# Optimization experiments

Hardware: AMD Instinct MI355X
Metric: run time of the kernel (lower is better)

The kernel has to match this reference:

```python
import math
import jax, jax.numpy as jnp
import numpy as np

DIM = 1024
DIM_HEAD = 64
NUM_HEAD = 16
HIDDEN = DIM_HEAD * NUM_HEAD  # 1024
B, L = 4, 2048
EPS = 1e-12  # torch F.normalize eps


def rms_norm(x, g):
    # F.normalize(x, dim=-1) * g * sqrt(d): L2-normalize then rescale
    d = x.shape[-1]
    norm = jnp.maximum(jnp.linalg.norm(x, axis=-1, keepdims=True), EPS)
    return x / norm * g * math.sqrt(d)


def setup_inputs() -> dict:
    key = jax.random.key(0)
    ks = jax.random.split(key, 8)
    x = jax.random.normal(ks[0], (B, L, DIM), dtype=jnp.float32)
    # torch Linear init scale ~ 1/sqrt(fan_in)
    s1 = 1.0 / math.sqrt(DIM)
    s2 = 1.0 / math.sqrt(HIDDEN)
    Wqkv = jax.random.uniform(ks[1], (3 * HIDDEN, DIM), minval=-s1, maxval=s1, dtype=jnp.float32)
    bqkv = jax.random.uniform(ks[2], (3 * HIDDEN,), minval=-s1, maxval=s1, dtype=jnp.float32)
    Wout = jax.random.uniform(ks[3], (DIM, HIDDEN), minval=-s2, maxval=s2, dtype=jnp.float32)
    bout = jax.random.uniform(ks[4], (DIM,), minval=-s2, maxval=s2, dtype=jnp.float32)
    g_q = jnp.ones((HIDDEN,), dtype=jnp.float32)
    g_k = jnp.ones((HIDDEN,), dtype=jnp.float32)
    g_out = jnp.ones((DIM,), dtype=jnp.float32)
    return {"x": x, "Wqkv": Wqkv, "bqkv": bqkv, "Wout": Wout, "bout": bout,
            "g_q": g_q, "g_k": g_k, "g_out": g_out}


def reference(x, Wqkv, bqkv, Wout, bout, g_q, g_k, g_out):
    scale = DIM_HEAD ** -0.5
    qkv = x @ Wqkv.T + bqkv  # (b, l, 3*hidden)
    q, k, v = jnp.split(qkv, 3, axis=-1)
    # QK RMSNorm applied over flattened (num_head*d) channel dim
    q = rms_norm(q, g_q)
    k = rms_norm(k, g_k)
    split_heads = lambda t: t.reshape(B, L, NUM_HEAD, DIM_HEAD).transpose(0, 2, 1, 3)
    q, k, v = split_heads(q), split_heads(k), split_heads(v)  # (b, h, l, d)
    q = q * scale
    sim = jnp.einsum('bhld,bhnd->bhln', q, k)
    attn = jax.nn.softmax(sim, axis=-1)
    out = jnp.einsum('bhln,bhnd->bhld', attn, v)  # (b, h, l, d)
    out = out.transpose(0, 2, 1, 3).reshape(B, L, HIDDEN)  # b l (h d)
    out = out @ Wout.T + bout
    return rms_norm(out, g_out)
```

## Files before the change

### kernel.cpp

```cpp
#include <hip/hip_runtime.h>
#include <math.h>

#define DIM       1024
#define DIM_HEAD  64
#define NUM_HEAD  16
#define HIDDEN    1024
#define BATCH     4
#define SEQ       2048
#define ROWS      (BATCH * SEQ)
#define QKV_N     (3 * HIDDEN)
#define QK_N      2048

typedef __bf16 bf16_t;
typedef __bf16 bf16x8 __attribute__((ext_vector_type(8)));
typedef __bf16 bf16x4 __attribute__((ext_vector_type(4)));
typedef float  f32x4  __attribute__((ext_vector_type(4)));

#define F32_ONE_PATTERN 0x3F800000u
#define LOG2E 1.44269504088896f

#define GLOAD_LDS16(gp, lp)                                                  \
    __builtin_amdgcn_global_load_lds(                                        \
        (const __attribute__((address_space(1))) void*)(const void*)(gp),    \
        (__attribute__((address_space(3))) void*)(void*)(lp), 16, 0, 0)

__global__ __launch_bounds__(256) void decode_all(
    const void* __restrict__ x_raw,    const void* __restrict__ wqkv_raw,
    const void* __restrict__ wout_raw, const void* __restrict__ bqkv_raw,
    const void* __restrict__ bout_raw, const void* __restrict__ gq_raw,
    const void* __restrict__ gk_raw,   const void* __restrict__ gout_raw,
    bf16_t* __restrict__ xb, bf16_t* __restrict__ wqkvb, bf16_t* __restrict__ woutb,
    float* __restrict__ o_bqkv, float* __restrict__ o_bout,
    float* __restrict__ o_gq,   float* __restrict__ o_gk,
    float* __restrict__ o_gout,
    const unsigned* __restrict__ sniff)
{
    const bool isf32 = (*sniff == F32_ONE_PATTERN);
    const int blk = blockIdx.x;
    if (blk < 6144) {
        const void* src; bf16_t* dst; long base;
        if (blk < 4096)      { src = x_raw;    dst = xb;    base = (long)blk * 2048; }
        else if (blk < 5632) { src = wqkv_raw; dst = wqkvb; base = (long)(blk - 4096) * 2048; }
        else                 { src = wout_raw; dst = woutb; base = (long)(blk - 5632) * 2048; }
        const long i = base + threadIdx.x * 8;
        if (isf32) {
            const float* p = (const float*)src + i;
            f32x4 a = *(const f32x4*)p;
            f32x4 b = *(const f32x4*)(p + 4);
            bf16x8 r;
            r[0] = (bf16_t)a[0]; r[1] = (bf16_t)a[1]; r[2] = (bf16_t)a[2]; r[3] = (bf16_t)a[3];
            r[4] = (bf16_t)b[0]; r[5] = (bf16_t)b[1]; r[6] = (bf16_t)b[2]; r[7] = (bf16_t)b[3];
            *(bf16x8*)&dst[i] = r;
        } else {
            *(bf16x8*)&dst[i] = *(const bf16x8*)((const bf16_t*)src + i);
        }
    } else {
        const int pb = blk - 6144;
        const void* src; float* dst; int off;
        if (pb < 3)       { src = bqkv_raw; dst = o_bqkv; off = pb * 1024; }
        else if (pb == 3) { src = bout_raw; dst = o_bout; off = 0; }
        else if (pb == 4) { src = gq_raw;   dst = o_gq;   off = 0; }
        else if (pb == 5) { src = gk_raw;   dst = o_gk;   off = 0; }
        else              { src = gout_raw; dst = o_gout; off = 0; }
        const int i = off + threadIdx.x * 4;
        if (isf32) {
            *(f32x4*)&dst[i] = *((const f32x4*)src + (off >> 2) + threadIdx.x);
        } else {
            bf16x4 v = *((const bf16x4*)src + (off >> 2) + threadIdx.x);
            f32x4 a;
            a[0] = (float)v[0]; a[1] = (float)v[1]; a[2] = (float)v[2]; a[3] = (float)v[3];
            *(f32x4*)&dst[i] = a;
        }
    }
}

__global__ __launch_bounds__(256) void gemm_qkv(
    const bf16_t* __restrict__ A,
    const bf16_t* __restrict__ Bt,
    const float*  __restrict__ bias,
    bf16_t* __restrict__ qk,
    bf16_t* __restrict__ vt)
{
    __shared__ __align__(16) bf16_t smem[16384];
    bf16_t* const As = smem;
    bf16_t* const Bs = smem + 8192;
    bf16_t* const Ts = smem;

    const int tid  = threadIdx.x;
    const int w    = tid >> 6;
    const int lane = tid & 63;
    const int wr   = w >> 1;
    const int wc   = w & 1;
    const int lr   = lane & 15;
    const int quad = lane >> 4;

    int lid = blockIdx.y * 24 + blockIdx.x;
    lid = (lid & 7) * 192 + (lid >> 3);
    const int bx = lid % 24, by = lid / 24;
    const int m0 = by * 128;
    const int n0 = bx * 128;
    const int K  = DIM;

    const int r    = tid >> 3;
    const int cswz = (((tid & 7) * 16) ^ ((r & 7) << 4)) >> 1;

    const int fsw0 = (quad * 8) ^ ((lr & 7) << 3);
    const int fsw1 = (32 + quad * 8) ^ ((lr & 7) << 3);

    f32x4 acc[4][4];
    #pragma unroll
    for (int i = 0; i < 4; i++)
        #pragma unroll
        for (int j = 0; j < 4; j++)
            acc[i][j] = (f32x4){0.f, 0.f, 0.f, 0.f};

    const bf16_t* pa = &A [(size_t)(m0 + r) * K + cswz];
    const bf16_t* pb = &Bt[(size_t)(n0 + r) * K + cswz];

    for (int k0 = 0; k0 < K; k0 += 64) {
        __syncthreads();
        #pragma unroll
        for (int p = 0; p < 4; p++) {
            GLOAD_LDS16(pa + (size_t)p * 32 * K + k0, &As[p * 2048 + tid * 8]);
            GLOAD_LDS16(pb + (size_t)p * 32 * K + k0, &Bs[p * 2048 + tid * 8]);
        }
        __syncthreads();

        bf16x8 af0[4], af1[4], bf0[4], bf1[4];
        #pragma unroll
        for (int i = 0; i < 4; i++) {
            const int row = (wr * 64 + i * 16 + lr) * 64;
            af0[i] = *(const bf16x8*)&As[row + fsw0];
            af1[i] = *(const bf16x8*)&As[row + fsw1];
        }
        #pragma unroll
        for (int j = 0; j < 4; j++) {
            const int row = (wc * 64 + j * 16 + lr) * 64;
            bf0[j] = *(const bf16x8*)&Bs[row + fsw0];
            bf1[j] = *(const bf16x8*)&Bs[row + fsw1];
        }
        #pragma unroll
        for (int i = 0; i < 4; i++)
            #pragma unroll
            for (int j = 0; j < 4; j++)
                acc[i][j] = __builtin_amdgcn_mfma_f32_16x16x32_bf16(
                    bf0[j], af0[i], acc[i][j], 0, 0, 0);
        #pragma unroll
        for (int i = 0; i < 4; i++)
            #pragma unroll
            for (int j = 0; j < 4; j++)
                acc[i][j] = __builtin_amdgcn_mfma_f32_16x16x32_bf16(
                    bf1[j], af1[i], acc[i][j], 0, 0, 0);
    }

    if (n0 < 2048) {
        #pragma unroll
        for (int i = 0; i < 4; i++) {
            const int row = m0 + wr * 64 + i * 16 + lr;
            #pragma unroll
            for (int j = 0; j < 4; j++) {
                const int col = n0 + wc * 64 + j * 16 + quad * 4;
                f32x4 bv = *(const f32x4*)&bias[col];
                f32x4 v = acc[i][j];
                bf16x4 o;
                o[0] = (bf16_t)(v[0] + bv[0]);
                o[1] = (bf16_t)(v[1] + bv[1]);
                o[2] = (bf16_t)(v[2] + bv[2]);
                o[3] = (bf16_t)(v[3] + bv[3]);
                *(bf16x4*)&qk[(size_t)row * QK_N + col] = o;
            }
        }
    } else {
        const int b      = m0 >> 11;
        const int l_base = m0 & 2047;
        const int c_base = n0 - 2048;
        #pragma unroll
        for (int p = 0; p < 2; p++) {
            __syncthreads();
            if (wc == p) {
                #pragma unroll
                for (int j = 0; j < 4; j++) {
                    const int cb = j * 16 + quad * 4;
                    f32x4 bv = *(const f32x4*)&bias[2048 + c_base + p * 64 + cb];
                    #pragma unroll
                    for (int i = 0; i < 4; i++) {
                        const int l = wr * 64 + i * 16 + lr;
                        f32x4 v = acc[i][j];
                        #pragma unroll
                        for (int rr = 0; rr < 4; rr++)
                            Ts[(cb + rr) * 136 + l] = (bf16_t)(v[rr] + bv[rr]);
                    }
                }
            }
            __syncthreads();
            const int c2 = tid >> 2, li = (tid & 3) * 32;
            const int cg = c_base + p * 64 + c2;
            const int h = cg >> 6, d = cg & 63;
            bf16_t* vrow = vt + ((size_t)((b << 4) | h) * 64 + d) * SEQ + l_base + li;
            #pragma unroll
            for (int e = 0; e < 4; e++)
                *(bf16x8*)&vrow[e * 8] = *(const bf16x8*)&Ts[c2 * 136 + li + e * 8];
        }
    }
}

__global__ __launch_bounds__(256) void gemm_out(
    const bf16_t* __restrict__ A,
    const bf16_t* __restrict__ Bt,
    const float*  __restrict__ bias,
    bf16_t* __restrict__ C)
{
    __shared__ __align__(16) bf16_t As[128 * 64];
    __shared__ __align__(16) bf16_t Bs[128 * 64];

    const int tid  = threadIdx.x;
    const int w    = tid >> 6;
    const int lane = tid & 63;
    const int wr   = w >> 1;
    const int wc   = w & 1;
    const int lr   = lane & 15;
    const int quad = lane >> 4;

    int lid = blockIdx.y * 8 + blockIdx.x;
    lid = (lid & 7) * 64 + (lid >> 3);
    const int bx = lid & 7, by = lid >> 3;
    const int m0 = by * 128;
    const int n0 = bx * 128;
    const int K  = HIDDEN;
    const int N  = DIM;

    const int r    = tid >> 3;
    const int cswz = (((tid & 7) * 16) ^ ((r & 7) << 4)) >> 1;
    const int fsw0 = (quad * 8) ^ ((lr & 7) << 3);
    const int fsw1 = (32 + quad * 8) ^ ((lr & 7) << 3);

    f32x4 acc[4][4];
    #pragma unroll
    for (int i = 0; i < 4; i++)
        #pragma unroll
        for (int j = 0; j < 4; j++)
            acc[i][j] = (f32x4){0.f, 0.f, 0.f, 0.f};

    const bf16_t* pa = &A [(size_t)(m0 + r) * K + cswz];
    const bf16_t* pb = &Bt[(size_t)(n0 + r) * K + cswz];

    for (int k0 = 0; k0 < K; k0 += 64) {
        __syncthreads();
        #pragma unroll
        for (int p = 0; p < 4; p++) {
            GLOAD_LDS16(pa + (size_t)p * 32 * K + k0, &As[p * 2048 + tid * 8]);
            GLOAD_LDS16(pb + (size_t)p * 32 * K + k0, &Bs[p * 2048 + tid * 8]);
        }
        __syncthreads();

        bf16x8 af0[4], af1[4], bf0[4], bf1[4];
        #pragma unroll
        for (int i = 0; i < 4; i++) {
            const int row = (wr * 64 + i * 16 + lr) * 64;
            af0[i] = *(const bf16x8*)&As[row + fsw0];
            af1[i] = *(const bf16x8*)&As[row + fsw1];
        }
        #pragma unroll
        for (int j = 0; j < 4; j++) {
            const int row = (wc * 64 + j * 16 + lr) * 64;
            bf0[j] = *(const bf16x8*)&Bs[row + fsw0];
            bf1[j] = *(const bf16x8*)&Bs[row + fsw1];
        }
        #pragma unroll
        for (int i = 0; i < 4; i++)
            #pragma unroll
            for (int j = 0; j < 4; j++)
                acc[i][j] = __builtin_amdgcn_mfma_f32_16x16x32_bf16(
                    bf0[j], af0[i], acc[i][j], 0, 0, 0);
        #pragma unroll
        for (int i = 0; i < 4; i++)
            #pragma unroll
            for (int j = 0; j < 4; j++)
                acc[i][j] = __builtin_amdgcn_mfma_f32_16x16x32_bf16(
                    bf1[j], af1[i], acc[i][j], 0, 0, 0);
    }

    #pragma unroll
    for (int i = 0; i < 4; i++) {
        const int row = m0 + wr * 64 + i * 16 + lr;
        #pragma unroll
        for (int j = 0; j < 4; j++) {
            const int col = n0 + wc * 64 + j * 16 + quad * 4;
            f32x4 bv = *(const f32x4*)&bias[col];
            f32x4 v = acc[i][j];
            bf16x4 o;
            o[0] = (bf16_t)(v[0] + bv[0]);
            o[1] = (bf16_t)(v[1] + bv[1]);
            o[2] = (bf16_t)(v[2] + bv[2]);
            o[3] = (bf16_t)(v[3] + bv[3]);
            *(bf16x4*)&C[(size_t)row * N + col] = o;
        }
    }
}

__device__ __forceinline__ void norm_apply(bf16_t* __restrict__ row,
                                           const float* __restrict__ g,
                                           float mult, int tid, float* red)
{
    bf16x4 xv = *(const bf16x4*)&row[tid * 4];
    float f0 = (float)xv[0], f1 = (float)xv[1], f2 = (float)xv[2], f3 = (float)xv[3];
    float ss = f0 * f0 + f1 * f1 + f2 * f2 + f3 * f3;
    #pragma unroll
    for (int off = 32; off > 0; off >>= 1) ss += __shfl_xor(ss, off, 64);
    if ((tid & 63) == 0) red[tid >> 6] = ss;
    __syncthreads();
    const float tot  = red[0] + red[1] + red[2] + red[3];
    const float fac  = mult / fmaxf(sqrtf(tot), 1e-12f);
    f32x4 gv = *(const f32x4*)&g[tid * 4];
    bf16x4 o;
    o[0] = (bf16_t)(f0 * gv[0] * fac);
    o[1] = (bf16_t)(f1 * gv[1] * fac);
    o[2] = (bf16_t)(f2 * gv[2] * fac);
    o[3] = (bf16_t)(f3 * gv[3] * fac);
    *(bf16x4*)&row[tid * 4] = o;
    __syncthreads();
}

__global__ __launch_bounds__(256) void qk_rmsnorm(bf16_t* __restrict__ qk,
                                                  const float* __restrict__ gq,
                                                  const float* __restrict__ gk)
{
    __shared__ float red[4];
    const size_t base = (size_t)blockIdx.x * QK_N;
    norm_apply(qk + base, gq, 4.0f * LOG2E, threadIdx.x, red);
    norm_apply(qk + base + HIDDEN, gk, 32.0f, threadIdx.x, red);
}

__global__ __launch_bounds__(256) void final_rmsnorm(const bf16_t* __restrict__ in,
                                                     const float* __restrict__ g,
                                                     void* __restrict__ out,
                                                     const unsigned* __restrict__ sniff)
{
    __shared__ float red[4];
    const bool isf32 = (*sniff == F32_ONE_PATTERN);
    const int tid = threadIdx.x;
    const bf16_t* row = in + (size_t)blockIdx.x * HIDDEN;

    bf16x4 xv = *(const bf16x4*)&row[tid * 4];
    float f0 = (float)xv[0], f1 = (float)xv[1], f2 = (float)xv[2], f3 = (float)xv[3];
    float ss = f0 * f0 + f1 * f1 + f2 * f2 + f3 * f3;
    #pragma unroll
    for (int off = 32; off > 0; off >>= 1) ss += __shfl_xor(ss, off, 64);
    if ((tid & 63) == 0) red[tid >> 6] = ss;
    __syncthreads();
    const float tot = red[0] + red[1] + red[2] + red[3];
    const float fac = 32.0f / fmaxf(sqrtf(tot), 1e-12f);
    f32x4 gv = *(const f32x4*)&g[tid * 4];
    f32x4 o;
    o[0] = f0 * gv[0] * fac;
    o[1] = f1 * gv[1] * fac;
    o[2] = f2 * gv[2] * fac;
    o[3] = f3 * gv[3] * fac;
    if (isf32) {
        *(f32x4*)((float*)out + (size_t)blockIdx.x * HIDDEN + tid * 4) = o;
    } else {
        bf16x4 ob;
        ob[0] = (bf16_t)o[0]; ob[1] = (bf16_t)o[1];
        ob[2] = (bf16_t)o[2]; ob[3] = (bf16_t)o[3];
        *(bf16x4*)((bf16_t*)out + (size_t)blockIdx.x * HIDDEN + tid * 4) = ob;
    }
}

__global__ __launch_bounds__(256) void attn_mfma9(const bf16_t* __restrict__ qk,
                                                  const bf16_t* __restrict__ vt,
                                                  bf16_t* __restrict__ out)
{
    __shared__ __align__(16) bf16_t Ks[4][2][2048];
    __shared__ __align__(16) union {
        bf16_t Ps[4][64 * 40];
        float  Obuf[2][64][68];
    } sh;
    __shared__ float lred[4][4][16];

    const int tid  = threadIdx.x;
    const int w    = tid >> 6;
    const int lane = tid & 63;
    const int l15  = lane & 15;
    const int quad = lane >> 4;

    const int j    = blockIdx.x;
    const int xcd  = j & 7;
    const int slot = j >> 3;
    const int bh   = ((slot >> 5) << 3) | xcd;
    const int q0   = (slot & 31) * 64;
    const int b = bh >> 4, h = bh & 15;

    bf16x8 qf[4][2];
    #pragma unroll
    for (int qt = 0; qt < 4; qt++) {
        const bf16_t* qrow = qk + (size_t)(b * SEQ + q0 + qt * 16 + l15) * QK_N + h * DIM_HEAD;
        qf[qt][0] = *(const bf16x8*)&qrow[quad * 8];
        qf[qt][1] = *(const bf16x8*)&qrow[32 + quad * 8];
    }

    f32x4 O[4][4];
    float lp[4] = {0.f, 0.f, 0.f, 0.f};
    #pragma unroll
    for (int qt = 0; qt < 4; qt++)
        #pragma unroll
        for (int dt = 0; dt < 4; dt++)
            O[qt][dt] = (f32x4){0.f, 0.f, 0.f, 0.f};

    const int r8  = lane >> 3;
    const int c8l = lane & 7;
    const int srccol = ((c8l * 8 + (r8 & 3) * 16) & 63);
    const bf16_t* kstage = qk + (size_t)(b * SEQ + w * 32) * QK_N + HIDDEN + h * DIM_HEAD
                         + r8 * QK_N + srccol;
    bf16_t* const ksb = &Ks[w][0][0];

    const int swz0 = ((quad * 8 + 64 - (l15 & 3) * 16) & 63);
    const int swz1 = ((32 + quad * 8 + 64 - (l15 & 3) * 16) & 63);
    const int krow = l15 * 64;

    #pragma unroll
    for (int t = 0; t < 4; t++)
        GLOAD_LDS16(kstage + t * 8 * QK_N, ksb + t * 512);
    kstage += 128 * QK_N;

    const bf16_t* vptr = vt + (size_t)bh * 64 * SEQ + w * 32;
    const int voff = l15 * SEQ + quad * 8;
    bf16_t* const psw = sh.Ps[w] + l15 * 40 + quad * 4;
    const bf16_t* const psr = sh.Ps[w] + l15 * 40 + quad * 8;

    for (int it = 0; it < SEQ / 128; it++) {
        const int cur = (it & 1) * 2048;
        const int nxt = 2048 - cur;
        __builtin_amdgcn_s_waitcnt(0x0F70);

        bf16x8 vB[4];
        #pragma unroll
        for (int dt = 0; dt < 4; dt++)
            vB[dt] = *(const bf16x8*)(vptr + voff + dt * 16 * SEQ);
        vptr += 128;

        bf16x8 kA[2][2];
        kA[0][0] = *(const bf16x8*)&ksb[cur + krow + swz0];
        kA[0][1] = *(const bf16x8*)&ksb[cur + krow + swz1];
        kA[1][0] = *(const bf16x8*)&ksb[cur + 1024 + krow + swz0];
        kA[1][1] = *(const bf16x8*)&ksb[cur + 1024 + krow + swz1];

        #pragma unroll
        for (int t = 0; t < 4; t++)
            GLOAD_LDS16(kstage + t * 8 * QK_N, ksb + nxt + t * 512);
        kstage += 128 * QK_N;

        f32x4 s[2][4];
        #pragma unroll
        for (int kt = 0; kt < 2; kt++)
            #pragma unroll
            for (int qt = 0; qt < 4; qt++) {
                f32x4 z = (f32x4){0.f, 0.f, 0.f, 0.f};
                z = __builtin_amdgcn_mfma_f32_16x16x32_bf16(kA[kt][0], qf[qt][0], z, 0, 0, 0);
                s[kt][qt] = __builtin_amdgcn_mfma_f32_16x16x32_bf16(kA[kt][1], qf[qt][1], z, 0, 0, 0);
            }

        #pragma unroll
        for (int qt = 0; qt < 4; qt++)
            #pragma unroll
            for (int kt = 0; kt < 2; kt++) {
                bf16x4 pk;
                #pragma unroll
                for (int r = 0; r < 4; r++) {
                    const float p = __builtin_amdgcn_exp2f(s[kt][qt][r]);
                    lp[qt] += p;
                    pk[r] = (bf16_t)p;
                }
                *(bf16x4*)(psw + qt * 640 + kt * 16) = pk;
            }
        __builtin_amdgcn_s_waitcnt(0xC07F);

        #pragma unroll
        for (int qt = 0; qt < 4; qt++) {
            bf16x8 pf = *(const bf16x8*)(psr + qt * 640);
            #pragma unroll
            for (int dt = 0; dt < 4; dt++)
                O[qt][dt] = __builtin_amdgcn_mfma_f32_16x16x32_bf16(pf, vB[dt], O[qt][dt], 0, 0, 0);
        }
    }

    #pragma unroll
    for (int qt = 0; qt < 4; qt++) {
        lp[qt] += __shfl_xor(lp[qt], 16, 64);
        lp[qt] += __shfl_xor(lp[qt], 32, 64);
    }
    __syncthreads();
    if (w >= 2) {
        #pragma unroll
        for (int qt = 0; qt < 4; qt++)
            #pragma unroll
            for (int dt = 0; dt < 4; dt++)
                #pragma unroll
                for (int r = 0; r < 4; r++)
                    sh.Obuf[w - 2][qt * 16 + quad * 4 + r][dt * 16 + l15] = O[qt][dt][r];
    }
    if (quad == 0) {
        #pragma unroll
        for (int qt = 0; qt < 4; qt++) lred[w][qt][l15] = lp[qt];
    }
    __syncthreads();
    if (w < 2) {
        #pragma unroll
        for (int qt = 0; qt < 4; qt++)
            #pragma unroll
            for (int dt = 0; dt < 4; dt++)
                #pragma unroll
                for (int r = 0; r < 4; r++) {
                    float* p = &sh.Obuf[w][qt * 16 + quad * 4 + r][dt * 16 + l15];
                    *p += O[qt][dt][r];
                }
    }
    __syncthreads();
    #pragma unroll
    for (int i = 0; i < 2; i++) {
        const int u   = tid + i * 256;
        const int row = u >> 3;
        const int c8  = (u & 7) * 8;
        const float ls = lred[0][row >> 4][row & 15] + lred[1][row >> 4][row & 15]
                       + lred[2][row >> 4][row & 15] + lred[3][row >> 4][row & 15];
        const float inv = 1.0f / ls;
        f32x4 a0 = *(const f32x4*)&sh.Obuf[0][row][c8];
        f32x4 a1 = *(const f32x4*)&sh.Obuf[0][row][c8 + 4];
        f32x4 b0 = *(const f32x4*)&sh.Obuf[1][row][c8];
        f32x4 b1 = *(const f32x4*)&sh.Obuf[1][row][c8 + 4];
        bf16x8 o;
        o[0] = (bf16_t)((a0[0] + b0[0]) * inv);
        o[1] = (bf16_t)((a0[1] + b0[1]) * inv);
        o[2] = (bf16_t)((a0[2] + b0[2]) * inv);
        o[3] = (bf16_t)((a0[3] + b0[3]) * inv);
        o[4] = (bf16_t)((a1[0] + b1[0]) * inv);
        o[5] = (bf16_t)((a1[1] + b1[1]) * inv);
        o[6] = (bf16_t)((a1[2] + b1[2]) * inv);
        o[7] = (bf16_t)((a1[3] + b1[3]) * inv);
        *(bf16x8*)&out[(size_t)(b * SEQ + q0 + row) * HIDDEN + h * DIM_HEAD + c8] = o;
    }
}

extern "C" void kernel_launch(void* const* d_in, const int* in_sizes, int n_in,
                              void* d_out, int out_size, void* d_ws, size_t ws_size,
                              hipStream_t stream)
{
    (void)in_sizes; (void)n_in; (void)out_size; (void)ws_size;
    const void* x_raw    = d_in[0];
    const void* Wqkv_raw = d_in[1];
    const void* bqkv_raw = d_in[2];
    const void* Wout_raw = d_in[3];
    const void* bout_raw = d_in[4];
    const void* gq_raw   = d_in[5];
    const void* gk_raw   = d_in[6];
    const void* gout_raw = d_in[7];
    const unsigned* sniff = (const unsigned*)d_in[5];

    char* ws = (char*)d_ws;
    bf16_t* xb      = (bf16_t*)(ws + 0);
    bf16_t* Wqkvb   = (bf16_t*)(ws + (16l << 20));
    bf16_t* Woutb   = (bf16_t*)(ws + (22l << 20));
    float*  bqkv_f  = (float*) (ws + (24l << 20));
    float*  bout_f  = (float*) (ws + (24l << 20) + 16384);
    float*  gq_f    = (float*) (ws + (24l << 20) + 2 * 16384);
    float*  gk_f    = (float*) (ws + (24l << 20) + 3 * 16384);
    float*  gout_f  = (float*) (ws + (24l << 20) + 4 * 16384);
    bf16_t* qk      = (bf16_t*)(ws + (25l << 20));
    bf16_t* vtb     = (bf16_t*)(ws + (57l << 20));
    bf16_t* attn_o  = xb;
    bf16_t* out_b   = qk;

    decode_all<<<6151, 256, 0, stream>>>(
        x_raw, Wqkv_raw, Wout_raw, bqkv_raw, bout_raw, gq_raw, gk_raw, gout_raw,
        xb, Wqkvb, Woutb, bqkv_f, bout_f, gq_f, gk_f, gout_f, sniff);

    gemm_qkv<<<dim3(QKV_N / 128, ROWS / 128), 256, 0, stream>>>(
        xb, Wqkvb, bqkv_f, qk, vtb);
    qk_rmsnorm<<<ROWS, 256, 0, stream>>>(qk, gq_f, gk_f);
    attn_mfma9<<<(SEQ / 64) * BATCH * NUM_HEAD, 256, 0, stream>>>(qk, vtb, attn_o);
    gemm_out<<<dim3(DIM / 128, ROWS / 128), 256, 0, stream>>>(
        attn_o, Woutb, bout_f, out_b);
    final_rmsnorm<<<ROWS, 256, 0, stream>>>(out_b, gout_f, d_out, sniff);
}
```

Baseline: 308.8 us.

## Double-buffer LDS tiles in QKV and output GEMMs to overlap loads with MFMA

Both projection GEMMs now use two LDS buffers (64 KB total) and issue the direct global-to-LDS loads for the next K tile before computing on the current one. Partial vmcnt waits plus raw s_barrier replace the two __syncthreads per iteration, so global memory latency can hide behind the MFMA work. The cost is double the shared memory, which may lower occupancy. It also relies on manual waitcnt counting being correct for the async LDS loads.

```diff
diff --git a/kernel.cpp b/kernel.cpp
--- a/kernel.cpp
+++ b/kernel.cpp
@@ -81,9 +81,7 @@
     bf16_t* __restrict__ qk,
     bf16_t* __restrict__ vt)
 {
-    __shared__ __align__(16) bf16_t smem[16384];
-    bf16_t* const As = smem;
-    bf16_t* const Bs = smem + 8192;
+    __shared__ __align__(16) bf16_t smem[32768];
     bf16_t* const Ts = smem;
 
     const int tid  = threadIdx.x;
@@ -103,7 +101,6 @@
 
     const int r    = tid >> 3;
     const int cswz = (((tid & 7) * 16) ^ ((r & 7) << 4)) >> 1;
-
     const int fsw0 = (quad * 8) ^ ((lr & 7) << 3);
     const int fsw1 = (32 + quad * 8) ^ ((lr & 7) << 3);
 
@@ -117,27 +114,41 @@
     const bf16_t* pa = &A [(size_t)(m0 + r) * K + cswz];
     const bf16_t* pb = &Bt[(size_t)(n0 + r) * K + cswz];
 
-    for (int k0 = 0; k0 < K; k0 += 64) {
-        __syncthreads();
-        #pragma unroll
-        for (int p = 0; p < 4; p++) {
-            GLOAD_LDS16(pa + (size_t)p * 32 * K + k0, &As[p * 2048 + tid * 8]);
-            GLOAD_LDS16(pb + (size_t)p * 32 * K + k0, &Bs[p * 2048 + tid * 8]);
-        }
-        __syncthreads();
+    #pragma unroll
+    for (int p = 0; p < 4; p++) {
+        GLOAD_LDS16(pa + (size_t)p * 32 * K, &smem[p * 2048 + tid * 8]);
+        GLOAD_LDS16(pb + (size_t)p * 32 * K, &smem[8192 + p * 2048 + tid * 8]);
+    }
+
+    const int NT = K / 64;
+    for (int t = 0; t < NT; t++) {
+        const int cur = (t & 1) * 16384;
+        const int nxt = 16384 - cur;
+        if (t + 1 < NT) {
+            const size_t koff = (size_t)(t + 1) * 64;
+            #pragma unroll
+            for (int p = 0; p < 4; p++) {
+                GLOAD_LDS16(pa + (size_t)p * 32 * K + koff, &smem[nxt + p * 2048 + tid * 8]);
+                GLOAD_LDS16(pb + (size_t)p * 32 * K + koff, &smem[nxt + 8192 + p * 2048 + tid * 8]);
+            }
+            asm volatile("s_waitcnt vmcnt(8)" ::: "memory");
+        } else {
+            asm volatile("s_waitcnt vmcnt(0)" ::: "memory");
+        }
+        __builtin_amdgcn_s_barrier();
 
         bf16x8 af0[4], af1[4], bf0[4], bf1[4];
         #pragma unroll
         for (int i = 0; i < 4; i++) {
-            const int row = (wr * 64 + i * 16 + lr) * 64;
-            af0[i] = *(const bf16x8*)&As[row + fsw0];
-            af1[i] = *(const bf16x8*)&As[row + fsw1];
+            const int row = cur + (wr * 64 + i * 16 + lr) * 64;
+            af0[i] = *(const bf16x8*)&smem[row + fsw0];
+            af1[i] = *(const bf16x8*)&smem[row + fsw1];
         }
         #pragma unroll
         for (int j = 0; j < 4; j++) {
-            const int row = (wc * 64 + j * 16 + lr) * 64;
-            bf0[j] = *(const bf16x8*)&Bs[row + fsw0];
-            bf1[j] = *(const bf16x8*)&Bs[row + fsw1];
+            const int row = cur + 8192 + (wc * 64 + j * 16 + lr) * 64;
+            bf0[j] = *(const bf16x8*)&smem[row + fsw0];
+            bf1[j] = *(const bf16x8*)&smem[row + fsw1];
         }
         #pragma unroll
         for (int i = 0; i < 4; i++)
@@ -151,6 +162,7 @@
             for (int j = 0; j < 4; j++)
                 acc[i][j] = __builtin_amdgcn_mfma_f32_16x16x32_bf16(
                     bf1[j], af1[i], acc[i][j], 0, 0, 0);
+        __builtin_amdgcn_s_barrier();
     }
 
     if (n0 < 2048) {
@@ -210,8 +222,7 @@
     const float*  __restrict__ bias,
     bf16_t* __restrict__ C)
 {
-    __shared__ __align__(16) bf16_t As[128 * 64];
-    __shared__ __align__(16) bf16_t Bs[128 * 64];
+    __shared__ __align__(16) bf16_t smem[32768];
 
     const int tid  = threadIdx.x;
     const int w    = tid >> 6;
@@ -244,27 +255,41 @@
     const bf16_t* pa = &A [(size_t)(m0 + r) * K + cswz];
     const bf16_t* pb = &Bt[(size_t)(n0 + r) * K + cswz];
 
-    for (int k0 = 0; k0 < K; k0 += 64) {
-        __syncthreads();
-        #pragma unroll
-        for (int p = 0; p < 4; p++) {
-            GLOAD_LDS16(pa + (size_t)p * 32 * K + k0, &As[p * 2048 + tid * 8]);
-            GLOAD_LDS16(pb + (size_t)p * 32 * K + k0, &Bs[p * 2048 + tid * 8]);
-        }
-        __syncthreads();
+    #pragma unroll
+    for (int p = 0; p < 4; p++) {
+        GLOAD_LDS16(pa + (size_t)p * 32 * K, &smem[p * 2048 + tid * 8]);
+        GLOAD_LDS16(pb + (size_t)p * 32 * K, &smem[8192 + p * 2048 + tid * 8]);
+    }
+
+    const int NT = K / 64;
+    for (int t = 0; t < NT; t++) {
+        const int cur = (t & 1) * 16384;
+        const int nxt = 16384 - cur;
+        if (t + 1 < NT) {
+            const size_t koff = (size_t)(t + 1) * 64;
+            #pragma unroll
+            for (int p = 0; p < 4; p++) {
+                GLOAD_LDS16(pa + (size_t)p * 32 * K + koff, &smem[nxt + p * 2048 + tid * 8]);
+                GLOAD_LDS16(pb + (size_t)p * 32 * K + koff, &smem[nxt + 8192 + p * 2048 + tid * 8]);
+            }
+            asm volatile("s_waitcnt vmcnt(8)" ::: "memory");
+        } else {
+            asm volatile("s_waitcnt vmcnt(0)" ::: "memory");
+        }
+        __builtin_amdgcn_s_barrier();
 
         bf16x8 af0[4], af1[4], bf0[4], bf1[4];
         #pragma unroll
         for (int i = 0; i < 4; i++) {
-            const int row = (wr * 64 + i * 16 + lr) * 64;
-            af0[i] = *(const bf16x8*)&As[row + fsw0];
-            af1[i] = *(const bf16x8*)&As[row + fsw1];
+            const int row = cur + (wr * 64 + i * 16 + lr) * 64;
+            af0[i] = *(const bf16x8*)&smem[row + fsw0];
+            af1[i] = *(const bf16x8*)&smem[row + fsw1];
         }
         #pragma unroll
         for (int j = 0; j < 4; j++) {
-            const int row = (wc * 64 + j * 16 + lr) * 64;
-            bf0[j] = *(const bf16x8*)&Bs[row + fsw0];
-            bf1[j] = *(const bf16x8*)&Bs[row + fsw1];
+            const int row = cur + 8192 + (wc * 64 + j * 16 + lr) * 64;
+            bf0[j] = *(const bf16x8*)&smem[row + fsw0];
+            bf1[j] = *(const bf16x8*)&smem[row + fsw1];
         }
         #pragma unroll
         for (int i = 0; i < 4; i++)
@@ -278,6 +303,7 @@
             for (int j = 0; j < 4; j++)
                 acc[i][j] = __builtin_amdgcn_mfma_f32_16x16x32_bf16(
                     bf1[j], af1[i], acc[i][j], 0, 0, 0);
+        __builtin_amdgcn_s_barrier();
     }
 
     #pragma unroll
```

Result: slower. 334.1 us (+8.2%).

## Triple-buffer GEMM K-loop with async LDS loads and vmcnt-based waits

Applied to the files above, without the earlier changes.

Both the QKV and output projection GEMMs move from a single-buffered 64-wide K step with two barriers per iteration to a three-stage ring of 32-wide K tiles. Loads for tile t+2 are issued before computing tile t, and partial vmcnt waits plus one barrier per step let global-to-LDS traffic overlap MFMA work. The swizzle changes to a 4-chunk XOR pattern for 32-element rows. In exchange, LDS use per block rises, which may lower occupancy, and the number of K iterations doubles.

```diff
diff --git a/kernel.cpp b/kernel.cpp
--- a/kernel.cpp
+++ b/kernel.cpp
@@ -81,9 +81,7 @@
     bf16_t* __restrict__ qk,
     bf16_t* __restrict__ vt)
 {
-    __shared__ __align__(16) bf16_t smem[16384];
-    bf16_t* const As = smem;
-    bf16_t* const Bs = smem + 8192;
+    __shared__ __align__(16) bf16_t smem[24576];
     bf16_t* const Ts = smem;
 
     const int tid  = threadIdx.x;
@@ -101,11 +99,9 @@
     const int n0 = bx * 128;
     const int K  = DIM;
 
-    const int r    = tid >> 3;
-    const int cswz = (((tid & 7) * 16) ^ ((r & 7) << 4)) >> 1;
-
-    const int fsw0 = (quad * 8) ^ ((lr & 7) << 3);
-    const int fsw1 = (32 + quad * 8) ^ ((lr & 7) << 3);
+    const int r    = tid >> 2;
+    const int cswz = (((tid & 3) ^ (r & 3)) * 8);
+    const int fsw  = ((quad ^ (lr & 3)) * 8);
 
     f32x4 acc[4][4];
     #pragma unroll
@@ -117,41 +113,55 @@
     const bf16_t* pa = &A [(size_t)(m0 + r) * K + cswz];
     const bf16_t* pb = &Bt[(size_t)(n0 + r) * K + cswz];
 
-    for (int k0 = 0; k0 < K; k0 += 64) {
-        __syncthreads();
-        #pragma unroll
-        for (int p = 0; p < 4; p++) {
-            GLOAD_LDS16(pa + (size_t)p * 32 * K + k0, &As[p * 2048 + tid * 8]);
-            GLOAD_LDS16(pb + (size_t)p * 32 * K + k0, &Bs[p * 2048 + tid * 8]);
-        }
-        __syncthreads();
-
-        bf16x8 af0[4], af1[4], bf0[4], bf1[4];
+#define QKV_STAGE(boff, kt)                                                   \
+    do {                                                                      \
+        const int ko = (kt) * 32;                                             \
+        GLOAD_LDS16(pa + ko,              &smem[(boff) + tid * 8]);           \
+        GLOAD_LDS16(pa + 64 * K + ko,     &smem[(boff) + 2048 + tid * 8]);    \
+        GLOAD_LDS16(pb + ko,              &smem[(boff) + 4096 + tid * 8]);    \
+        GLOAD_LDS16(pb + 64 * K + ko,     &smem[(boff) + 6144 + tid * 8]);    \
+    } while (0)
+
+    const int NT = K / 32;
+    QKV_STAGE(0, 0);
+    QKV_STAGE(8192, 1);
+    asm volatile("s_waitcnt vmcnt(4)" ::: "memory");
+    __builtin_amdgcn_s_barrier();
+
+    int curoff = 0;
+    for (int t = 0; t < NT; t++) {
+        if (t + 2 < NT) {
+            int stoff = curoff + 16384;
+            if (stoff >= 24576) stoff -= 24576;
+            QKV_STAGE(stoff, t + 2);
+        }
+        bf16x8 af[4], bfr[4];
         #pragma unroll
         for (int i = 0; i < 4; i++) {
-            const int row = (wr * 64 + i * 16 + lr) * 64;
-            af0[i] = *(const bf16x8*)&As[row + fsw0];
-            af1[i] = *(const bf16x8*)&As[row + fsw1];
+            const int row = wr * 64 + i * 16 + lr;
+            af[i] = *(const bf16x8*)&smem[curoff + row * 32 + fsw];
         }
         #pragma unroll
         for (int j = 0; j < 4; j++) {
-            const int row = (wc * 64 + j * 16 + lr) * 64;
-            bf0[j] = *(const bf16x8*)&Bs[row + fsw0];
-            bf1[j] = *(const bf16x8*)&Bs[row + fsw1];
+            const int row = wc * 64 + j * 16 + lr;
+            bfr[j] = *(const bf16x8*)&smem[curoff + 4096 + row * 32 + fsw];
         }
         #pragma unroll
         for (int i = 0; i < 4; i++)
             #pragma unroll
             for (int j = 0; j < 4; j++)
                 acc[i][j] = __builtin_amdgcn_mfma_f32_16x16x32_bf16(
-                    bf0[j], af0[i], acc[i][j], 0, 0, 0);
-        #pragma unroll
-        for (int i = 0; i < 4; i++)
-            #pragma unroll
-            for (int j = 0; j < 4; j++)
-                acc[i][j] = __builtin_amdgcn_mfma_f32_16x16x32_bf16(
-                    bf1[j], af1[i], acc[i][j], 0, 0, 0);
-    }
+                    bfr[j], af[i], acc[i][j], 0, 0, 0);
+        if (t + 2 < NT) {
+            asm volatile("s_waitcnt vmcnt(4)" ::: "memory");
+        } else {
+            asm volatile("s_waitcnt vmcnt(0)" ::: "memory");
+        }
+        __builtin_amdgcn_s_barrier();
+        curoff += 8192;
+        if (curoff == 24576) curoff = 0;
+    }
+#undef QKV_STAGE
 
     if (n0 < 2048) {
         #pragma unroll
@@ -210,8 +220,7 @@
     const float*  __restrict__ bias,
     bf16_t* __restrict__ C)
 {
-    __shared__ __align__(16) bf16_t As[128 * 64];
-    __shared__ __align__(16) bf16_t Bs[128 * 64];
+    __shared__ __align__(16) bf16_t smem[24576];
 
     const int tid  = threadIdx.x;
     const int w    = tid >> 6;
@@ -229,10 +238,9 @@
     const int K  = HIDDEN;
     const int N  = DIM;
 
-    const int r    = tid >> 3;
-    const int cswz = (((tid & 7) * 16) ^ ((r & 7) << 4)) >> 1;
-    const int fsw0 = (quad * 8) ^ ((lr & 7) << 3);
-    const int fsw1 = (32 + quad * 8) ^ ((lr & 7) << 3);
+    const int r    = tid >> 2;
+    const int cswz = (((tid & 3) ^ (r & 3)) * 8);
+    const int fsw  = ((quad ^ (lr & 3)) * 8);
 
     f32x4 acc[4][4];
     #pragma unroll
@@ -244,41 +252,55 @@
     const bf16_t* pa = &A [(size_t)(m0 + r) * K + cswz];
     const bf16_t* pb = &Bt[(size_t)(n0 + r) * K + cswz];
 
-    for (int k0 = 0; k0 < K; k0 += 64) {
-        __syncthreads();
-        #pragma unroll
-        for (int p = 0; p < 4; p++) {
-            GLOAD_LDS16(pa + (size_t)p * 32 * K + k0, &As[p * 2048 + tid * 8]);
-            GLOAD_LDS16(pb + (size_t)p * 32 * K + k0, &Bs[p * 2048 + tid * 8]);
-        }
-        __syncthreads();
-
-        bf16x8 af0[4], af1[4], bf0[4], bf1[4];
+#define OUT_STAGE(boff, kt)                                                   \
+    do {                                                                      \
+        const int ko = (kt) * 32;                                             \
+        GLOAD_LDS16(pa + ko,              &smem[(boff) + tid * 8]);           \
+        GLOAD_LDS16(pa + 64 * K + ko,     &smem[(boff) + 2048 + tid * 8]);    \
+        GLOAD_LDS16(pb + ko,              &smem[(boff) + 4096 + tid * 8]);    \
+        GLOAD_LDS16(pb + 64 * K + ko,     &smem[(boff) + 6144 + tid * 8]);    \
+    } while (0)
+
+    const int NT = K / 32;
+    OUT_STAGE(0, 0);
+    OUT_STAGE(8192, 1);
+    asm volatile("s_waitcnt vmcnt(4)" ::: "memory");
+    __builtin_amdgcn_s_barrier();
+
+    int curoff = 0;
+    for (int t = 0; t < NT; t++) {
+        if (t + 2 < NT) {
+            int stoff = curoff + 16384;
+            if (stoff >= 24576) stoff -= 24576;
+            OUT_STAGE(stoff, t + 2);
+        }
+        bf16x8 af[4], bfr[4];
         #pragma unroll
         for (int i = 0; i < 4; i++) {
-            const int row = (wr * 64 + i * 16 + lr) * 64;
-            af0[i] = *(const bf16x8*)&As[row + fsw0];
-            af1[i] = *(const bf16x8*)&As[row + fsw1];
+            const int row = wr * 64 + i * 16 + lr;
+            af[i] = *(const bf16x8*)&smem[curoff + row * 32 + fsw];
         }
         #pragma unroll
         for (int j = 0; j < 4; j++) {
-            const int row = (wc * 64 + j * 16 + lr) * 64;
-            bf0[j] = *(const bf16x8*)&Bs[row + fsw0];
-            bf1[j] = *(const bf16x8*)&Bs[row + fsw1];
+            const int row = wc * 64 + j * 16 + lr;
+            bfr[j] = *(const bf16x8*)&smem[curoff + 4096 + row * 32 + fsw];
         }
         #pragma unroll
         for (int i = 0; i < 4; i++)
             #pragma unroll
             for (int j = 0; j < 4; j++)
                 acc[i][j] = __builtin_amdgcn_mfma_f32_16x16x32_bf16(
-                    bf0[j], af0[i], acc[i][j], 0, 0, 0);
-        #pragma unroll
-        for (int i = 0; i < 4; i++)
-            #pragma unroll
-            for (int j = 0; j < 4; j++)
-                acc[i][j] = __builtin_amdgcn_mfma_f32_16x16x32_bf16(
-                    bf1[j], af1[i], acc[i][j], 0, 0, 0);
-    }
+                    bfr[j], af[i], acc[i][j], 0, 0, 0);
+        if (t + 2 < NT) {
+            asm volatile("s_waitcnt vmcnt(4)" ::: "memory");
+        } else {
+            asm volatile("s_waitcnt vmcnt(0)" ::: "memory");
+        }
+        __builtin_amdgcn_s_barrier();
+        curoff += 8192;
+        if (curoff == 24576) curoff = 0;
+    }
+#undef OUT_STAGE
 
     #pragma unroll
     for (int i = 0; i < 4; i++) {
```

Result: slower. 321.6 us (+4.1%).
